# Kernel tuning notes

Hardware: AMD Instinct MI355X
Metric: run time of the kernel (lower is better)

## Reference

```python
import jax, jax.numpy as jnp
import numpy as np

B, N, C = 8, 100000, 90          # batch, total anchors over all levels, num_classes (COCO)
SCORE_THR = 0.05                  # pre_nms_score_threshold
IOU_THR = 0.5                     # nms_iou_threshold
MAX_DET = 100                     # max_num_detections (per class and total)
PRE_NMS_K = 512                   # per-class candidate cap before greedy NMS
NEG = -1e9                        # suppressed-score sentinel


def setup_inputs() -> dict:
    key = jax.random.key(0)
    kb, ks = jax.random.split(key)
    raw = jax.random.uniform(kb, (B, N, 1, 4), dtype=jnp.float32) * 512.0
    # build valid [y1, x1, y2, x2] boxes from the rand fill
    y1 = jnp.minimum(raw[..., 0], raw[..., 2])
    y2 = jnp.maximum(raw[..., 0], raw[..., 2])
    x1 = jnp.minimum(raw[..., 1], raw[..., 3])
    x2 = jnp.maximum(raw[..., 1], raw[..., 3])
    boxes = jnp.stack([y1, x1, y2, x2], axis=-1)            # [B, N, 1, 4]
    scores = jax.random.uniform(ks, (B, N, C), dtype=jnp.float32)  # [B, N, C]
    return {"boxes": boxes, "scores": scores}


def _iou_one_vs_all(box, boxes):
    # box: [4], boxes: [K, 4], layout (y1, x1, y2, x2)
    yy1 = jnp.maximum(box[0], boxes[:, 0])
    xx1 = jnp.maximum(box[1], boxes[:, 1])
    yy2 = jnp.minimum(box[2], boxes[:, 2])
    xx2 = jnp.minimum(box[3], boxes[:, 3])
    inter = jnp.clip(yy2 - yy1, 0.0) * jnp.clip(xx2 - xx1, 0.0)
    area = (box[2] - box[0]) * (box[3] - box[1])
    areas = (boxes[:, 2] - boxes[:, 0]) * (boxes[:, 3] - boxes[:, 1])
    return inter / (area + areas - inter + 1e-8)


def _nms_single(cboxes, cscores):
    # Greedy per-class NMS: cboxes [K,4], cscores [K] -> MAX_DET boxes/scores.
    K = cboxes.shape[0]
    idxs = jnp.arange(K)

    def step(active, _):
        j = jnp.argmax(active)
        s = active[j]
        b = cboxes[j]
        iou = _iou_one_vs_all(b, cboxes)
        sup = (iou > IOU_THR) | (idxs == j)
        return jnp.where(sup, NEG, active), (b, s)

    _, (sel_boxes, sel_scores) = jax.lax.scan(step, cscores, None, length=MAX_DET)
    return sel_boxes, sel_scores  # [MAX_DET, 4], [MAX_DET]


def _detections(boxes, scores):
    bx = boxes[:, :, 0, :]                                   # class-agnostic boxes [B, N, 4]
    sm = jnp.where(scores >= SCORE_THR, scores, NEG)         # score thresholding
    st = jnp.transpose(sm, (0, 2, 1))                        # [B, C, N]
    cscores, cidx = jax.lax.top_k(st, PRE_NMS_K)             # [B, C, K]
    cboxes = jax.vmap(lambda b, i: b[i])(bx, cidx)           # [B, C, K, 4]
    sel_boxes, sel_scores = jax.vmap(jax.vmap(_nms_single))(cboxes, cscores)
    cls = jnp.broadcast_to(jnp.arange(C)[None, :, None], (B, C, MAX_DET))
    fs = sel_scores.reshape(B, -1)                           # [B, C*MAX_DET]
    fb = sel_boxes.reshape(B, -1, 4)
    fc = cls.reshape(B, -1)
    top_s, top_i = jax.lax.top_k(fs, MAX_DET)                # top MAX_DET over all classes
    top_b = jnp.take_along_axis(fb, top_i[..., None], axis=1)
    top_c = jnp.take_along_axis(fc, top_i, axis=1)
    valid = top_s >= SCORE_THR
    out_boxes = jnp.where(valid[..., None], top_b, 0.0)     # [B, MAX_DET, 4]
    out_scores = jnp.where(valid, top_s, 0.0)               # [B, MAX_DET]
    out_classes = jnp.where(valid, top_c, 0).astype(jnp.int32)
    num_valid = valid.sum(axis=1).astype(jnp.int32)         # [B]
    return out_boxes, out_scores, out_classes, num_valid


def reference(boxes, scores):
    return _detections(boxes, scores)
```

## Files before the change

### kernel.cpp

```cpp
#include <hip/hip_runtime.h>

#define NB 8
#define NN 100000
#define NC 90
#define SCORE_THR 0.05f
#define IOU_THR 0.5f
#define MAX_DET 100
#define PRE_NMS_K 512
#define NEGV -1000000000.0f
#define T0 0.9925f
#define CAP 1024
#define NBC (NB * NC)
#define CNT_STRIDE 16
#define CHUNK 1024
#define NCHUNK 98
#define LCAP 32
#define IOU_CMP_C 0x1.0000008p-1

__device__ __forceinline__ unsigned ordf(float s) {
    unsigned u = __float_as_uint(s);
    return (u & 0x80000000u) ? ~u : (u | 0x80000000u);
}
__device__ __forceinline__ float deordf(unsigned o) {
    return (o & 0x80000000u) ? __uint_as_float(o ^ 0x80000000u) : __uint_as_float(~o);
}
__device__ __forceinline__ unsigned long long mkkey(float s, unsigned idx) {
    return ((unsigned long long)ordf(s) << 32) | (unsigned long long)(0xFFFFFFFFu - idx);
}

__global__ __launch_bounds__(256) void k_zero(uint4* __restrict__ cnt4, uint4* __restrict__ ovf4) {
    unsigned i = blockIdx.x * 256u + threadIdx.x;
    if (i < (NBC * CNT_STRIDE) / 4) cnt4[i] = make_uint4(0u, 0u, 0u, 0u);
    if (i < NBC / 4) ovf4[i] = make_uint4(0u, 0u, 0u, 0u);
}

__global__ __launch_bounds__(512) void k_collect(const float* __restrict__ scores,
                                                 unsigned* __restrict__ cnt,
                                                 unsigned* __restrict__ ovf,
                                                 unsigned long long* __restrict__ buf) {
    __shared__ unsigned long long lst[NC][LCAP + 1];
    __shared__ unsigned lcnt[NC];
    int b = blockIdx.x / NCHUNK;
    int chunk = blockIdx.x - b * NCHUNK;
    int n0 = chunk * CHUNK;
    int ncount = NN - n0; if (ncount > CHUNK) ncount = CHUNK;
    int nf4 = (ncount * NC) >> 2;
    const float4* base4 = reinterpret_cast<const float4*>(scores + ((size_t)b * NN + n0) * NC);

    for (int i = threadIdx.x; i < NC; i += 512) lcnt[i] = 0u;
    __syncthreads();

    for (int i = threadIdx.x; i < nf4; i += 512) {
        float4 v = base4[i];
        float ss[4] = {v.x, v.y, v.z, v.w};
        #pragma unroll
        for (int e = 0; e < 4; ++e) {
            if (ss[e] >= T0) {
                int local = 4 * i + e;
                int c = local % NC;
                int n = n0 + local / NC;
                unsigned slot = atomicAdd(&lcnt[c], 1u);
                if (slot < LCAP) lst[c][slot] = mkkey(ss[e], (unsigned)n);
                else atomicOr(&ovf[b * NC + c], 1u);
            }
        }
    }
    __syncthreads();

    if (threadIdx.x < NC) {
        int c = threadIdx.x;
        unsigned k = lcnt[c]; if (k > LCAP) k = LCAP;
        if (k) {
            int bc = b * NC + c;
            unsigned basep = atomicAdd(&cnt[(size_t)bc * CNT_STRIDE], k);
            if (basep + k > CAP) atomicOr(&ovf[bc], 1u);
            unsigned lim = (basep + k <= CAP) ? k : (basep < CAP ? CAP - basep : 0u);
            for (unsigned j = 0; j < lim; ++j)
                buf[(size_t)bc * CAP + basep + j] = lst[c][j];
        }
    }
}

__global__ __launch_bounds__(256) void k_sortnms(const float* __restrict__ scores,
                                                 const float* __restrict__ boxes,
                                                 const unsigned* __restrict__ cnt,
                                                 const unsigned* __restrict__ ovf,
                                                 const unsigned long long* __restrict__ buf,
                                                 float* __restrict__ sel_score,
                                                 float4* __restrict__ sel_box) {
    #pragma clang fp contract(off)
    int bc = blockIdx.x;
    int tid = threadIdx.x;
    __shared__ unsigned long long keys[CAP];
    __shared__ float4 box_lds[PRE_NMS_K];
    __shared__ float area_lds[PRE_NMS_K];
    __shared__ unsigned hist[1024];
    __shared__ unsigned s_lcnt;
    __shared__ float s_cut;

    unsigned K = cnt[(size_t)bc * CNT_STRIDE];
    bool bad = (ovf[bc] != 0u) || (K < (unsigned)PRE_NMS_K) || (K > CAP);

    if (bad) {
        int b = bc / NC, c = bc - (bc / NC) * NC;
        for (int i = tid; i < 1024; i += 256) hist[i] = 0u;
        if (tid == 0) s_lcnt = 0u;
        __syncthreads();
        for (int n = tid; n < NN; n += 256) {
            float s = scores[((size_t)b * NN + n) * NC + c];
            if (s >= SCORE_THR) {
                int bin = (int)(s * 1024.0f);
                bin = bin < 0 ? 0 : (bin > 1023 ? 1023 : bin);
                atomicAdd(&hist[bin], 1u);
            }
        }
        __syncthreads();
        if (tid == 0) {
            unsigned tot = 0;
            for (int i = 0; i < 1024; ++i) tot += hist[i];
            unsigned target = tot < (unsigned)PRE_NMS_K ? tot : (unsigned)PRE_NMS_K;
            float cut = 3.0e38f;
            if (target > 0) {
                unsigned cum = 0; int t = 1023;
                for (; t >= 0; --t) { cum += hist[t]; if (cum >= target) break; }
                cut = (float)t / 1024.0f;
                if (cut < SCORE_THR) cut = SCORE_THR;
            }
            s_cut = cut;
        }
        __syncthreads();
        float cut = s_cut;
        for (int n = tid; n < NN; n += 256) {
            float s = scores[((size_t)b * NN + n) * NC + c];
            if (s >= SCORE_THR && s >= cut) {
                unsigned slot = atomicAdd(&s_lcnt, 1u);
                if (slot < CAP) keys[slot] = mkkey(s, (unsigned)n);
            }
        }
        __syncthreads();
        K = s_lcnt; if (K > CAP) K = CAP;
        for (unsigned i = K + tid; i < CAP; i += 256) keys[i] = 0ULL;
        __syncthreads();
    } else {
        for (unsigned i = tid; i < CAP; i += 256)
            keys[i] = (i < K) ? buf[(size_t)bc * CAP + i] : 0ULL;
    }

    bool prev_big = false;
    for (unsigned k2 = 2; k2 <= CAP; k2 <<= 1) {
        for (unsigned j = k2 >> 1; j; j >>= 1) {
            bool big = (j >= 64);
            if (big || prev_big) __syncthreads();
            #pragma unroll
            for (unsigned ii = 0; ii < 4; ++ii) {
                unsigned i = tid + ii * 256u;
                unsigned ixj = i ^ j;
                if (ixj > i) {
                    unsigned long long a = keys[i], bv = keys[ixj];
                    bool desc = ((i & k2) == 0);
                    if (desc ? (a < bv) : (a > bv)) { keys[i] = bv; keys[ixj] = a; }
                }
            }
            prev_big = big;
        }
    }
    __syncthreads();

    int b = bc / NC;
    for (int r = tid; r < PRE_NMS_K; r += 256) {
        unsigned long long key = keys[r];
        float4 bx = make_float4(0.f, 0.f, 0.f, 0.f);
        if (key != 0ULL) {
            unsigned n = 0xFFFFFFFFu - (unsigned)(key & 0xFFFFFFFFu);
            bx = *reinterpret_cast<const float4*>(boxes + ((size_t)b * NN + n) * 4);
        }
        box_lds[r] = bx;
        area_lds[r] = (bx.z - bx.x) * (bx.w - bx.y);
    }
    __syncthreads();

    if (tid < 64) {
        int lane = tid;
        float y1[8], x1[8], y2[8], x2[8], ar[8];
        unsigned alive = 0u;
        #pragma unroll
        for (int k = 0; k < 8; ++k) {
            int r = lane * 8 + k;
            float4 bx = box_lds[r];
            y1[k] = bx.x; x1[k] = bx.y; y2[k] = bx.z; x2[k] = bx.w;
            ar[k] = area_lds[r];
            if (keys[r] != 0ULL) alive |= (1u << k);
        }
        for (int it = 0; it < MAX_DET; ++it) {
            unsigned long long bal = __ballot(alive != 0u);
            if (bal == 0ULL) {
                if (lane == 0) {
                    sel_score[bc * MAX_DET + it] = NEGV;
                    sel_box[bc * MAX_DET + it] = make_float4(0.f, 0.f, 0.f, 0.f);
                }
                continue;
            }
            int lw = __ffsll((unsigned long long)bal) - 1;
            unsigned aw = __shfl(alive, lw);
            int bit = __ffs(aw) - 1;
            int widx = lw * 8 + bit;
            float4 wb = box_lds[widx];
            float warea = area_lds[widx];
            if (lane == 0) {
                unsigned long long wk = keys[widx];
                sel_score[bc * MAX_DET + it] = deordf((unsigned)(wk >> 32));
                sel_box[bc * MAX_DET + it] = wb;
            }
            unsigned sup = 0u;
            #pragma unroll
            for (int k = 0; k < 8; ++k) {
                float yy1 = fmaxf(wb.x, y1[k]);
                float xx1 = fmaxf(wb.y, x1[k]);
                float yy2 = fminf(wb.z, y2[k]);
                float xx2 = fminf(wb.w, x2[k]);
                float ih = fmaxf(yy2 - yy1, 0.0f);
                float iw = fmaxf(xx2 - xx1, 0.0f);
                float inter = ih * iw;
                float denom = ((warea + ar[k]) - inter) + 1e-8f;
                if ((double)inter > IOU_CMP_C * (double)denom) sup |= (1u << k);
            }
            alive &= ~sup;
            if (lane == lw) alive &= ~(1u << bit);
        }
    }
}

__global__ __launch_bounds__(64) void k_merge(const float* __restrict__ sel_score,
                                              const float4* __restrict__ sel_box,
                                              float* __restrict__ out) {
    int b = blockIdx.x;
    int lane = threadIdx.x;
    const float* ss = sel_score + b * NC * MAX_DET;
    __shared__ unsigned long long win[MAX_DET];
    int c1 = lane;
    int c2 = 64 + lane;
    int r1 = 0, r2 = 0;
    auto mk = [&](int c, int r) {
        float s = ss[c * MAX_DET + r];
        return mkkey(s, (unsigned)(c * MAX_DET + r));
    };
    unsigned long long k1 = mk(c1, 0);
    unsigned long long k2 = (lane < 26) ? mk(c2, 0) : 0ULL;
    for (int it = 0; it < MAX_DET; ++it) {
        unsigned long long w = k1 > k2 ? k1 : k2;
        for (int off = 1; off < 64; off <<= 1) {
            unsigned long long o = __shfl_xor(w, off);
            if (o > w) w = o;
        }
        if (lane == 0) win[it] = w;
        if (k1 == w) { r1++; k1 = (r1 < MAX_DET) ? mk(c1, r1) : 0ULL; }
        else if (lane < 26 && k2 == w) { r2++; k2 = (r2 < MAX_DET) ? mk(c2, r2) : 0ULL; }
    }
    __syncthreads();
    int nv = 0;
    for (int t = lane; t < MAX_DET; t += 64) {
        unsigned long long w = win[t];
        unsigned flat = 0xFFFFFFFFu - (unsigned)(w & 0xFFFFFFFFu);
        float sdec = deordf((unsigned)(w >> 32));
        bool valid = (w != 0ULL) && (sdec >= SCORE_THR);
        float4 bx = make_float4(0.f, 0.f, 0.f, 0.f);
        float so = 0.0f; int cls = 0;
        if (valid) {
            bx = sel_box[b * NC * MAX_DET + flat];
            so = sdec;
            cls = (int)(flat / MAX_DET);
            nv++;
        }
        float* ob = out + (size_t)(b * MAX_DET + t) * 4;
        ob[0] = bx.x; ob[1] = bx.y; ob[2] = bx.z; ob[3] = bx.w;
        out[NB * MAX_DET * 4 + b * MAX_DET + t] = so;
        out[NB * MAX_DET * 5 + b * MAX_DET + t] = (float)cls;
    }
    for (int off = 1; off < 64; off <<= 1) nv += __shfl_xor(nv, off);
    if (lane == 0) out[NB * MAX_DET * 6 + b] = (float)nv;
}

extern "C" void kernel_launch(void* const* d_in, const int* in_sizes, int n_in,
                              void* d_out, int out_size, void* d_ws, size_t ws_size,
                              hipStream_t stream) {
    const float* boxes = (const float*)d_in[0];
    const float* scores = (const float*)d_in[1];
    float* out = (float*)d_out;

    char* ws = (char*)d_ws;
    size_t off = 0;
    auto alloc = [&](size_t bytes) -> void* {
        void* p = ws + off;
        off = (off + bytes + 255) & ~(size_t)255;
        return p;
    };
    unsigned* cnt = (unsigned*)alloc((size_t)NBC * CNT_STRIDE * 4);
    unsigned* ovf = (unsigned*)alloc((size_t)NBC * 4);
    unsigned long long* buf = (unsigned long long*)alloc((size_t)NBC * CAP * 8);
    float* sel_score = (float*)alloc((size_t)NBC * MAX_DET * 4);
    float4* sel_box = (float4*)alloc((size_t)NBC * MAX_DET * 16);

    k_zero<<<(NBC * CNT_STRIDE / 4 + 255) / 256, 256, 0, stream>>>((uint4*)cnt, (uint4*)ovf);
    k_collect<<<NB * NCHUNK, 512, 0, stream>>>(scores, cnt, ovf, buf);
    k_sortnms<<<NBC, 256, 0, stream>>>(scores, boxes, cnt, ovf, buf, sel_score, sel_box);
    k_merge<<<NB, 64, 0, stream>>>(sel_score, sel_box, out);
}
```

Measured before the change: 182.2 us.

## Batch nontemporal score loads, alias NMS shared buffers, stage merge keys in LDS

Result: slower. 196.7 us (+8.0%).

```diff
diff --git a/kernel.cpp b/kernel.cpp
--- a/kernel.cpp
+++ b/kernel.cpp
@@ -17,6 +17,8 @@
 #define LCAP 32
 #define IOU_CMP_C 0x1.0000008p-1
 
+typedef float f32x4 __attribute__((ext_vector_type(4)));
+
 __device__ __forceinline__ unsigned ordf(float s) {
     unsigned u = __float_as_uint(s);
     return (u & 0x80000000u) ? ~u : (u | 0x80000000u);
@@ -45,23 +47,34 @@
     int n0 = chunk * CHUNK;
     int ncount = NN - n0; if (ncount > CHUNK) ncount = CHUNK;
     int nf4 = (ncount * NC) >> 2;
-    const float4* base4 = reinterpret_cast<const float4*>(scores + ((size_t)b * NN + n0) * NC);
+    const f32x4* base4 = reinterpret_cast<const f32x4*>(scores + ((size_t)b * NN + n0) * NC);
 
     for (int i = threadIdx.x; i < NC; i += 512) lcnt[i] = 0u;
     __syncthreads();
 
-    for (int i = threadIdx.x; i < nf4; i += 512) {
-        float4 v = base4[i];
-        float ss[4] = {v.x, v.y, v.z, v.w};
+    for (int i0 = (int)threadIdx.x; i0 < nf4; i0 += 2048) {
+        f32x4 v[4];
         #pragma unroll
-        for (int e = 0; e < 4; ++e) {
-            if (ss[e] >= T0) {
-                int local = 4 * i + e;
-                int c = local % NC;
-                int n = n0 + local / NC;
-                unsigned slot = atomicAdd(&lcnt[c], 1u);
-                if (slot < LCAP) lst[c][slot] = mkkey(ss[e], (unsigned)n);
-                else atomicOr(&ovf[b * NC + c], 1u);
+        for (int k = 0; k < 4; ++k) {
+            int idx = i0 + k * 512;
+            if (idx < nf4) v[k] = __builtin_nontemporal_load(base4 + idx);
+        }
+        #pragma unroll
+        for (int k = 0; k < 4; ++k) {
+            int idx = i0 + k * 512;
+            if (idx < nf4) {
+                #pragma unroll
+                for (int e = 0; e < 4; ++e) {
+                    float s = v[k][e];
+                    if (s >= T0) {
+                        int local = 4 * idx + e;
+                        int c = local % NC;
+                        int n = n0 + local / NC;
+                        unsigned slot = atomicAdd(&lcnt[c], 1u);
+                        if (slot < LCAP) lst[c][slot] = mkkey(s, (unsigned)n);
+                        else atomicOr(&ovf[b * NC + c], 1u);
+                    }
+                }
             }
         }
     }
@@ -92,9 +105,10 @@
     int bc = blockIdx.x;
     int tid = threadIdx.x;
     __shared__ unsigned long long keys[CAP];
-    __shared__ float4 box_lds[PRE_NMS_K];
-    __shared__ float area_lds[PRE_NMS_K];
-    __shared__ unsigned hist[1024];
+    __shared__ __align__(16) unsigned char gmem[PRE_NMS_K * 16 + PRE_NMS_K * 4];
+    float4* box_lds = (float4*)gmem;
+    float* area_lds = (float*)(gmem + PRE_NMS_K * 16);
+    unsigned* hist = (unsigned*)gmem;
     __shared__ unsigned s_lcnt;
     __shared__ float s_cut;
 
@@ -230,54 +244,57 @@
     }
 }
 
-__global__ __launch_bounds__(64) void k_merge(const float* __restrict__ sel_score,
-                                              const float4* __restrict__ sel_box,
-                                              float* __restrict__ out) {
+__global__ __launch_bounds__(256) void k_merge(const float* __restrict__ sel_score,
+                                               const float4* __restrict__ sel_box,
+                                               float* __restrict__ out) {
     int b = blockIdx.x;
-    int lane = threadIdx.x;
+    int tid = threadIdx.x;
+    __shared__ unsigned long long lkeys[NC * MAX_DET];
+    __shared__ unsigned long long win[MAX_DET];
     const float* ss = sel_score + b * NC * MAX_DET;
-    __shared__ unsigned long long win[MAX_DET];
-    int c1 = lane;
-    int c2 = 64 + lane;
-    int r1 = 0, r2 = 0;
-    auto mk = [&](int c, int r) {
-        float s = ss[c * MAX_DET + r];
-        return mkkey(s, (unsigned)(c * MAX_DET + r));
-    };
-    unsigned long long k1 = mk(c1, 0);
-    unsigned long long k2 = (lane < 26) ? mk(c2, 0) : 0ULL;
-    for (int it = 0; it < MAX_DET; ++it) {
-        unsigned long long w = k1 > k2 ? k1 : k2;
-        for (int off = 1; off < 64; off <<= 1) {
-            unsigned long long o = __shfl_xor(w, off);
-            if (o > w) w = o;
-        }
-        if (lane == 0) win[it] = w;
-        if (k1 == w) { r1++; k1 = (r1 < MAX_DET) ? mk(c1, r1) : 0ULL; }
-        else if (lane < 26 && k2 == w) { r2++; k2 = (r2 < MAX_DET) ? mk(c2, r2) : 0ULL; }
-    }
-    __syncthreads();
-    int nv = 0;
-    for (int t = lane; t < MAX_DET; t += 64) {
-        unsigned long long w = win[t];
-        unsigned flat = 0xFFFFFFFFu - (unsigned)(w & 0xFFFFFFFFu);
-        float sdec = deordf((unsigned)(w >> 32));
-        bool valid = (w != 0ULL) && (sdec >= SCORE_THR);
-        float4 bx = make_float4(0.f, 0.f, 0.f, 0.f);
-        float so = 0.0f; int cls = 0;
-        if (valid) {
-            bx = sel_box[b * NC * MAX_DET + flat];
-            so = sdec;
-            cls = (int)(flat / MAX_DET);
-            nv++;
-        }
-        float* ob = out + (size_t)(b * MAX_DET + t) * 4;
-        ob[0] = bx.x; ob[1] = bx.y; ob[2] = bx.z; ob[3] = bx.w;
-        out[NB * MAX_DET * 4 + b * MAX_DET + t] = so;
-        out[NB * MAX_DET * 5 + b * MAX_DET + t] = (float)cls;
-    }
-    for (int off = 1; off < 64; off <<= 1) nv += __shfl_xor(nv, off);
-    if (lane == 0) out[NB * MAX_DET * 6 + b] = (float)nv;
+
+    for (int i = tid; i < NC * MAX_DET; i += 256)
+        lkeys[i] = mkkey(ss[i], (unsigned)i);
+    __syncthreads();
+
+    if (tid < 64) {
+        int lane = tid;
+        int r1 = 0, r2 = 0;
+        unsigned long long k1 = lkeys[lane * MAX_DET];
+        unsigned long long k2 = (lane < 26) ? lkeys[(64 + lane) * MAX_DET] : 0ULL;
+        for (int it = 0; it < MAX_DET; ++it) {
+            unsigned long long w = k1 > k2 ? k1 : k2;
+            for (int off = 1; off < 64; off <<= 1) {
+                unsigned long long o = __shfl_xor(w, off);
+                if (o > w) w = o;
+            }
+            if (lane == 0) win[it] = w;
+            if (k1 == w) { r1++; k1 = (r1 < MAX_DET) ? lkeys[lane * MAX_DET + r1] : 0ULL; }
+            else if (lane < 26 && k2 == w) { r2++; k2 = (r2 < MAX_DET) ? lkeys[(64 + lane) * MAX_DET + r2] : 0ULL; }
+        }
+
+        int nv = 0;
+        for (int t = lane; t < MAX_DET; t += 64) {
+            unsigned long long w = win[t];
+            unsigned flat = 0xFFFFFFFFu - (unsigned)(w & 0xFFFFFFFFu);
+            float sdec = deordf((unsigned)(w >> 32));
+            bool valid = (w != 0ULL) && (sdec >= SCORE_THR);
+            float4 bx = make_float4(0.f, 0.f, 0.f, 0.f);
+            float so = 0.0f; int cls = 0;
+            if (valid) {
+                bx = sel_box[b * NC * MAX_DET + flat];
+                so = sdec;
+                cls = (int)(flat / MAX_DET);
+                nv++;
+            }
+            float* ob = out + (size_t)(b * MAX_DET + t) * 4;
+            ob[0] = bx.x; ob[1] = bx.y; ob[2] = bx.z; ob[3] = bx.w;
+            out[NB * MAX_DET * 4 + b * MAX_DET + t] = so;
+            out[NB * MAX_DET * 5 + b * MAX_DET + t] = (float)cls;
+        }
+        for (int off = 1; off < 64; off <<= 1) nv += __shfl_xor(nv, off);
+        if (lane == 0) out[NB * MAX_DET * 6 + b] = (float)nv;
+    }
 }
 
 extern "C" void kernel_launch(void* const* d_in, const int* in_sizes, int n_in,
@@ -303,5 +320,5 @@
     k_zero<<<(NBC * CNT_STRIDE / 4 + 255) / 256, 256, 0, stream>>>((uint4*)cnt, (uint4*)ovf);
     k_collect<<<NB * NCHUNK, 512, 0, stream>>>(scores, cnt, ovf, buf);
     k_sortnms<<<NBC, 256, 0, stream>>>(scores, boxes, cnt, ovf, buf, sel_score, sel_box);
-    k_merge<<<NB, 64, 0, stream>>>(sel_score, sel_box, out);
-}
+    k_merge<<<NB, 256, 0, stream>>>(sel_score, sel_box, out);
+}
```
